# Kernel tuning notes

Hardware: AMD Instinct MI355X
Metric: run time of the kernel (lower is better)

Reference implementation:

```python
import jax, jax.numpy as jnp
import numpy as np

B, S, H, NH, M = 2, 2048, 1024, 16, 512  # batch, seq, hidden, heads, medical/clinical dim
D = H // NH
EPS = 1e-12


def setup_inputs() -> dict:
    key = jax.random.key(0)
    ks = jax.random.split(key, 20)
    sd = 0.02
    return {
        'hidden_states': jax.random.normal(ks[0], (B, S, H), jnp.float32),
        'medical_context': jax.random.normal(ks[1], (B, S, H), jnp.float32),
        'Wq': jax.random.normal(ks[2], (H, H), jnp.float32) * sd,
        'bq': jnp.zeros((H,), jnp.float32),
        'Wk': jax.random.normal(ks[3], (H, H), jnp.float32) * sd,
        'bk': jnp.zeros((H,), jnp.float32),
        'Wv': jax.random.normal(ks[4], (H, H), jnp.float32) * sd,
        'bv': jnp.zeros((H,), jnp.float32),
        'Wmq': jax.random.normal(ks[5], (H, M), jnp.float32) * sd,
        'bmq': jnp.zeros((M,), jnp.float32),
        'Wmk': jax.random.normal(ks[6], (H, M), jnp.float32) * sd,
        'bmk': jnp.zeros((M,), jnp.float32),
        'Wc': jax.random.normal(ks[7], (H, M), jnp.float32) * sd,
        'bc': jnp.zeros((M,), jnp.float32),
        'Wf': jax.random.normal(ks[8], (H + M, H), jnp.float32) * sd,
        'bf': jnp.zeros((H,), jnp.float32),
        'ln_g': jnp.ones((H,), jnp.float32),
        'ln_b': jnp.zeros((H,), jnp.float32),
    }


def _split_heads(x):  # [B,S,H] -> [B,NH,S,D]
    return x.reshape(B, S, NH, D).transpose(0, 2, 1, 3)


def reference(hidden_states, medical_context, Wq, bq, Wk, bk, Wv, bv,
              Wmq, bmq, Wmk, bmk, Wc, bc, Wf, bf, ln_g, ln_b):
    hs = hidden_states
    q = _split_heads(hs @ Wq + bq)
    k = _split_heads(hs @ Wk + bk)
    v = _split_heads(hs @ Wv + bv)
    scores = jnp.einsum('bhsd,bhtd->bhst', q, k) / jnp.sqrt(jnp.float32(D))
    # medical additive bias
    mq = hs @ Wmq + bmq                      # [B,S,M]
    mk = medical_context @ Wmk + bmk         # [B,S,M]
    med_scores = jax.nn.softmax(jnp.einsum('bsm,btm->bst', mq, mk), axis=-1)
    scores = scores + 0.3 * med_scores[:, None]
    probs = jax.nn.softmax(scores, axis=-1)  # [B,NH,S,S]
    ctx = jnp.einsum('bhst,bhtd->bhsd', probs, v)
    ctx = ctx.transpose(0, 2, 1, 3).reshape(B, S, H)
    clin = ctx @ Wc + bc                     # [B,S,M]
    ctx = jnp.concatenate([ctx, clin], axis=-1) @ Wf + bf
    x = ctx + hs
    mu = jnp.mean(x, axis=-1, keepdims=True)
    var = jnp.mean(jnp.square(x - mu), axis=-1, keepdims=True)
    out = (x - mu) / jnp.sqrt(var + EPS) * ln_g + ln_b
    return out, probs
```

## Files before the change

kernel.cpp:

```cpp
#include <hip/hip_runtime.h>
#include <hip/hip_bf16.h>
#include <cstddef>

#define B_   2
#define S_   2048
#define H_   1024
#define NH_  16
#define D_   64
#define M_   512
#define NTOK (B_*S_)

typedef __hip_bfloat16 bf16;
typedef __attribute__((ext_vector_type(8))) short bf16x8;
typedef __attribute__((ext_vector_type(4))) float f32x4;
typedef __attribute__((ext_vector_type(8))) unsigned short ushort8;

__device__ __forceinline__ float toF(bf16 x) { return __bfloat162float(x); }
__device__ __forceinline__ float bfbits2f(unsigned short s) { return __uint_as_float((unsigned)s << 16); }
__device__ __forceinline__ unsigned short f2bfbits(float f) {
    union { bf16 h; unsigned short s; } u; u.h = __float2bfloat16(f); return u.s;
}

__global__ __launch_bounds__(256)
void detect_dtype(const unsigned int* __restrict__ w, int* __restrict__ flag)
{
    __shared__ int cnt[256];
    const int tid = threadIdx.x;
    const unsigned int x = w[tid];
    const unsigned int e0 = (x >> 7) & 0xFFu;
    cnt[tid] = (e0 >= 100u && e0 <= 126u) ? 1 : 0;
    __syncthreads();
    for (int off = 128; off > 0; off >>= 1) {
        if (tid < off) cnt[tid] += cnt[tid + off];
        __syncthreads();
    }
    if (tid == 0) flag[0] = (cnt[0] >= 128) ? 1 : 0;
}

__global__ __launch_bounds__(256)
void convert_in(const void* __restrict__ src, float* __restrict__ dst, int n,
                const int* __restrict__ flag)
{
    const int isbf = *flag;
    for (int i = blockIdx.x * 256 + threadIdx.x; i < n; i += gridDim.x * 256)
        dst[i] = isbf ? toF(((const bf16*)src)[i]) : ((const float*)src)[i];
}

__global__ __launch_bounds__(256)
void to_bf16_pack(const float* __restrict__ src, unsigned int* __restrict__ dst,
                  int n2)
{
    int i = blockIdx.x * 256 + threadIdx.x;
    const int stride = gridDim.x * 256;
    for (; i < n2; i += stride) {
        const float2 f = ((const float2*)src)[i];
        const unsigned int lo = f2bfbits(f.x);
        const unsigned int hi = f2bfbits(f.y);
        dst[i] = lo | (hi << 16);
    }
}

__global__ __launch_bounds__(256)
void gemm_tn(const float* __restrict__ A, const float* __restrict__ W,
             const float* __restrict__ bias, float* __restrict__ C,
             int M, int N, int K, int accumulate)
{
    __shared__ float As[16][68];
    __shared__ float Bs[16][68];
    const int tid = threadIdx.x;
    const int tx = tid & 15, ty = tid >> 4;
    const int m0 = blockIdx.y * 64, n0 = blockIdx.x * 64;
    float acc[4][4] = {};

    for (int k0 = 0; k0 < K; k0 += 16) {
        {
            const int r  = tid >> 2;
            const int cg = (tid & 3) * 4;
            const float* ap = A + (size_t)(m0 + r) * K + (k0 + cg);
            #pragma unroll
            for (int j = 0; j < 4; ++j) As[cg + j][r] = ap[j];
        }
        {
            const int r  = tid >> 4;
            const int cg = (tid & 15) * 4;
            const float* wp = W + (size_t)(k0 + r) * N + (n0 + cg);
            #pragma unroll
            for (int j = 0; j < 4; ++j) Bs[r][cg + j] = wp[j];
        }
        __syncthreads();
        #pragma unroll
        for (int kk = 0; kk < 16; ++kk) {
            float a[4], b[4];
            #pragma unroll
            for (int i = 0; i < 4; ++i) a[i] = As[kk][ty * 4 + i];
            #pragma unroll
            for (int j = 0; j < 4; ++j) b[j] = Bs[kk][tx * 4 + j];
            #pragma unroll
            for (int i = 0; i < 4; ++i)
                #pragma unroll
                for (int j = 0; j < 4; ++j)
                    acc[i][j] += a[i] * b[j];
        }
        __syncthreads();
    }

    #pragma unroll
    for (int i = 0; i < 4; ++i) {
        const int row = m0 + ty * 4 + i;
        #pragma unroll
        for (int j = 0; j < 4; ++j) {
            const int col = n0 + tx * 4 + j;
            float v = acc[i][j];
            if (bias) v += bias[col];
            const size_t idx = (size_t)row * N + col;
            if (accumulate) C[idx] += v; else C[idx] = v;
        }
    }
}

__global__ __launch_bounds__(256)
void med_logits(const float* __restrict__ mq, const float* __restrict__ mk,
                float* __restrict__ out)
{
    const int b = blockIdx.z;
    const float* A  = mq + (size_t)b * S_ * M_;
    const float* Bm = mk + (size_t)b * S_ * M_;
    __shared__ float As[16][68];
    __shared__ float Bs[16][68];
    const int tid = threadIdx.x;
    const int tx = tid & 15, ty = tid >> 4;
    const int m0 = blockIdx.y * 64, n0 = blockIdx.x * 64;
    float acc[4][4] = {};

    for (int k0 = 0; k0 < M_; k0 += 16) {
        const int r  = tid >> 2;
        const int cg = (tid & 3) * 4;
        const float* ap = A  + (size_t)(m0 + r) * M_ + (k0 + cg);
        const float* bp = Bm + (size_t)(n0 + r) * M_ + (k0 + cg);
        #pragma unroll
        for (int j = 0; j < 4; ++j) { As[cg + j][r] = ap[j]; Bs[cg + j][r] = bp[j]; }
        __syncthreads();
        #pragma unroll
        for (int kk = 0; kk < 16; ++kk) {
            float a[4], b[4];
            #pragma unroll
            for (int i = 0; i < 4; ++i) a[i] = As[kk][ty * 4 + i];
            #pragma unroll
            for (int j = 0; j < 4; ++j) b[j] = Bs[kk][tx * 4 + j];
            #pragma unroll
            for (int i = 0; i < 4; ++i)
                #pragma unroll
                for (int j = 0; j < 4; ++j)
                    acc[i][j] += a[i] * b[j];
        }
        __syncthreads();
    }
    #pragma unroll
    for (int i = 0; i < 4; ++i)
        #pragma unroll
        for (int j = 0; j < 4; ++j)
            out[(size_t)b * S_ * S_ + (size_t)(m0 + ty * 4 + i) * S_ + (n0 + tx * 4 + j)]
                = acc[i][j];
}

__global__ __launch_bounds__(256)
void row_softmax(float* __restrict__ x)
{
    float* p = x + (size_t)blockIdx.x * S_;
    __shared__ float red[256];
    const int tid = threadIdx.x;

    float m = -1e30f;
    for (int i = tid; i < S_; i += 256) m = fmaxf(m, p[i]);
    red[tid] = m; __syncthreads();
    for (int off = 128; off > 0; off >>= 1) {
        if (tid < off) red[tid] = fmaxf(red[tid], red[tid + off]);
        __syncthreads();
    }
    const float mx = red[0];
    __syncthreads();

    float s = 0.f;
    for (int i = tid; i < S_; i += 256) {
        float e = __expf(fmaxf(p[i] - mx, -80.f));
        p[i] = e; s += e;
    }
    red[tid] = s; __syncthreads();
    for (int off = 128; off > 0; off >>= 1) {
        if (tid < off) red[tid] += red[tid + off];
        __syncthreads();
    }
    const float inv = 1.f / fmaxf(red[0], 1e-30f);
    for (int i = tid; i < S_; i += 256) p[i] *= inv;
}

__global__ __launch_bounds__(256)
void qk_scores(const bf16* __restrict__ qh, const bf16* __restrict__ kh,
               const float* __restrict__ medp, void* __restrict__ dout,
               const int* __restrict__ flag)
{
    const int isbf = *flag;
    const int bh = blockIdx.z;
    const int b = bh >> 4;
    const int s0 = blockIdx.y * 64;
    const int t0 = blockIdx.x * 64;
    const int tid  = threadIdx.x;
    const int wave = tid >> 6, lane = tid & 63;
    const int wr = (wave >> 1) * 32, wc = (wave & 1) * 32;
    const int lr = lane & 15;
    const int lk = (lane >> 4) * 8;
    const int h  = bh & 15;

    const bf16* qp = qh + (size_t)(b * S_ + s0 + wr + lr) * H_ + h * D_ + lk;
    const bf16* kp = kh + (size_t)(b * S_ + t0 + wc + lr) * H_ + h * D_ + lk;

    f32x4 acc00 = {0.f, 0.f, 0.f, 0.f};
    f32x4 acc01 = acc00, acc10 = acc00, acc11 = acc00;

    #pragma unroll
    for (int ks = 0; ks < 2; ++ks) {
        const int d = ks * 32;
        const bf16x8 a0 = *(const bf16x8*)(qp + d);
        const bf16x8 a1 = *(const bf16x8*)(qp + (size_t)16 * H_ + d);
        const bf16x8 b0 = *(const bf16x8*)(kp + d);
        const bf16x8 b1 = *(const bf16x8*)(kp + (size_t)16 * H_ + d);
        acc00 = __builtin_amdgcn_mfma_f32_16x16x32_bf16(a0, b0, acc00, 0, 0, 0);
        acc01 = __builtin_amdgcn_mfma_f32_16x16x32_bf16(a0, b1, acc01, 0, 0, 0);
        acc10 = __builtin_amdgcn_mfma_f32_16x16x32_bf16(a1, b0, acc10, 0, 0, 0);
        acc11 = __builtin_amdgcn_mfma_f32_16x16x32_bf16(a1, b1, acc11, 0, 0, 0);
    }

    const size_t pbase = (size_t)NTOK * H_ + ((size_t)bh * S_ + s0) * S_ + t0;
    bf16*  ob = (bf16*)dout  + pbase;
    float* of = (float*)dout + pbase;
    const int crow = (lane >> 4) * 4;
    const int ccol = lane & 15;

    #pragma unroll
    for (int ti = 0; ti < 2; ++ti) {
        const f32x4 aT0 = ti ? acc10 : acc00;
        const f32x4 aT1 = ti ? acc11 : acc01;
        #pragma unroll
        for (int r = 0; r < 4; ++r) {
            const int row = wr + ti * 16 + crow + r;
            const float* mrow = medp + ((size_t)b * S_ + s0 + row) * S_ + t0;
            {
                const int col = wc + ccol;
                const float v = aT0[r] * 0.125f + 0.3f * mrow[col];
                if (isbf) ob[(size_t)row * S_ + col] = __float2bfloat16(v);
                else      of[(size_t)row * S_ + col] = v;
            }
            {
                const int col = wc + 16 + ccol;
                const float v = aT1[r] * 0.125f + 0.3f * mrow[col];
                if (isbf) ob[(size_t)row * S_ + col] = __float2bfloat16(v);
                else      of[(size_t)row * S_ + col] = v;
            }
        }
    }
}

__global__ __launch_bounds__(256)
void prob_softmax(void* __restrict__ dout, const int* __restrict__ flag)
{
    const int isbf = *flag;
    const int tid = threadIdx.x;
    const size_t base = (size_t)NTOK * H_ + (size_t)blockIdx.x * S_;
    __shared__ float red[256];
    float x[8];
    bf16*  pb = (bf16*)dout  + base;
    float* pf = (float*)dout + base;

    if (isbf) {
        const ushort8 v = *(const ushort8*)(pb + tid * 8);
        #pragma unroll
        for (int j = 0; j < 8; ++j) x[j] = bfbits2f(v[j]);
    } else {
        const float4 f0 = ((const float4*)pf)[tid * 2];
        const float4 f1 = ((const float4*)pf)[tid * 2 + 1];
        x[0] = f0.x; x[1] = f0.y; x[2] = f0.z; x[3] = f0.w;
        x[4] = f1.x; x[5] = f1.y; x[6] = f1.z; x[7] = f1.w;
    }

    float m = x[0];
    #pragma unroll
    for (int j = 1; j < 8; ++j) m = fmaxf(m, x[j]);
    red[tid] = m; __syncthreads();
    for (int off = 128; off > 0; off >>= 1) {
        if (tid < off) red[tid] = fmaxf(red[tid], red[tid + off]);
        __syncthreads();
    }
    const float mx = red[0];
    __syncthreads();

    float s = 0.f;
    #pragma unroll
    for (int j = 0; j < 8; ++j) {
        x[j] = __expf(fmaxf(x[j] - mx, -80.f));
        s += x[j];
    }
    red[tid] = s; __syncthreads();
    for (int off = 128; off > 0; off >>= 1) {
        if (tid < off) red[tid] += red[tid + off];
        __syncthreads();
    }
    const float inv = 1.f / fmaxf(red[0], 1e-30f);

    if (isbf) {
        ushort8 v;
        #pragma unroll
        for (int j = 0; j < 8; ++j) v[j] = f2bfbits(x[j] * inv);
        *(ushort8*)(pb + tid * 8) = v;
    } else {
        float4 f0, f1;
        f0.x = x[0] * inv; f0.y = x[1] * inv; f0.z = x[2] * inv; f0.w = x[3] * inv;
        f1.x = x[4] * inv; f1.y = x[5] * inv; f1.z = x[6] * inv; f1.w = x[7] * inv;
        ((float4*)pf)[tid * 2]     = f0;
        ((float4*)pf)[tid * 2 + 1] = f1;
    }
}

__global__ __launch_bounds__(256)
void pv_gemm(const void* __restrict__ dout, const float* __restrict__ v,
             float* __restrict__ ctx, const int* __restrict__ flag)
{
    const int isbf = *flag;
    const int bh = blockIdx.y;
    const int b = bh >> 4, h = bh & 15;
    const int m0 = blockIdx.x * 64;
    const size_t pbase = (size_t)NTOK * H_ + (size_t)bh * S_ * S_;
    const bf16*  Ab = (const bf16*)dout  + pbase;
    const float* Af = (const float*)dout + pbase;
    const float* Bv = v + (size_t)b * S_ * H_ + h * D_;
    __shared__ float As[16][68];
    __shared__ float Bs[16][68];
    const int tid = threadIdx.x;
    const int tx = tid & 15, ty = tid >> 4;
    float acc[4][4] = {};

    for (int k0 = 0; k0 < S_; k0 += 16) {
        {
            const int r  = tid >> 2;
            const int cg = (tid & 3) * 4;
            const size_t base = (size_t)(m0 + r) * S_ + (k0 + cg);
            #pragma unroll
            for (int j = 0; j < 4; ++j)
                As[cg + j][r] = isbf ? toF(Ab[base + j]) : Af[base + j];
        }
        {
            const int r  = tid >> 4;
            const int cg = (tid & 15) * 4;
            const float* bp = Bv + (size_t)(k0 + r) * H_ + cg;
            #pragma unroll
            for (int j = 0; j < 4; ++j) Bs[r][cg + j] = bp[j];
        }
        __syncthreads();
        #pragma unroll
        for (int kk = 0; kk < 16; ++kk) {
            float a[4], bb[4];
            #pragma unroll
            for (int i = 0; i < 4; ++i) a[i]  = As[kk][ty * 4 + i];
            #pragma unroll
            for (int j = 0; j < 4; ++j) bb[j] = Bs[kk][tx * 4 + j];
            #pragma unroll
            for (int i = 0; i < 4; ++i)
                #pragma unroll
                for (int j = 0; j < 4; ++j)
                    acc[i][j] += a[i] * bb[j];
        }
        __syncthreads();
    }
    #pragma unroll
    for (int i = 0; i < 4; ++i)
        #pragma unroll
        for (int j = 0; j < 4; ++j)
            ctx[(size_t)(b * S_ + m0 + ty * 4 + i) * H_ + h * D_ + tx * 4 + j] = acc[i][j];
}

__global__ __launch_bounds__(256)
void add_ln(const float* __restrict__ f, const float* __restrict__ hs,
            const float* __restrict__ g, const float* __restrict__ bta,
            void* __restrict__ dout, const int* __restrict__ flag)
{
    const int isbf = *flag;
    const int row = blockIdx.x;
    const int tid = threadIdx.x;
    __shared__ float red[256];
    float x[4];
    #pragma unroll
    for (int i = 0; i < 4; ++i) {
        const int c = tid + i * 256;
        x[i] = f[(size_t)row * H_ + c] + hs[(size_t)row * H_ + c];
    }
    float s = x[0] + x[1] + x[2] + x[3];
    red[tid] = s; __syncthreads();
    for (int off = 128; off > 0; off >>= 1) {
        if (tid < off) red[tid] += red[tid + off];
        __syncthreads();
    }
    const float mu = red[0] * (1.f / (float)H_);
    __syncthreads();

    float vs = 0.f;
    #pragma unroll
    for (int i = 0; i < 4; ++i) { const float d = x[i] - mu; vs += d * d; }
    red[tid] = vs; __syncthreads();
    for (int off = 128; off > 0; off >>= 1) {
        if (tid < off) red[tid] += red[tid + off];
        __syncthreads();
    }
    const float var = red[0] * (1.f / (float)H_);
    const float inv = 1.f / sqrtf(var + 1e-12f);
    bf16*  ob = (bf16*)dout;
    float* of = (float*)dout;
    #pragma unroll
    for (int i = 0; i < 4; ++i) {
        const int c = tid + i * 256;
        const float y = (x[i] - mu) * inv * g[c] + bta[c];
        if (isbf) ob[(size_t)row * H_ + c] = __float2bfloat16(y);
        else      of[(size_t)row * H_ + c] = y;
    }
}

extern "C" void kernel_launch(void* const* d_in, const int* in_sizes, int n_in,
                              void* d_out, int out_size, void* d_ws, size_t ws_size,
                              hipStream_t stream)
{
    int* flag = (int*)d_ws;
    float* p = (float*)((char*)d_ws + 256);

    float* hs_f  = p; p += (size_t)NTOK * H_;
    float* mc_f  = p; p += (size_t)NTOK * H_;
    float* Wq_f  = p; p += (size_t)H_ * H_;
    float* Wk_f  = p; p += (size_t)H_ * H_;
    float* Wv_f  = p; p += (size_t)H_ * H_;
    float* Wmq_f = p; p += (size_t)H_ * M_;
    float* Wmk_f = p; p += (size_t)H_ * M_;
    float* Wc_f  = p; p += (size_t)H_ * M_;
    float* Wf_f  = p; p += (size_t)(H_ + M_) * H_;
    float* bq_f  = p; p += H_;
    float* bk_f  = p; p += H_;
    float* bv_f  = p; p += H_;
    float* bmq_f = p; p += M_;
    float* bmk_f = p; p += M_;
    float* bc_f  = p; p += M_;
    float* bf_f  = p; p += H_;
    float* lng_f = p; p += H_;
    float* lnb_f = p; p += H_;

    float* q    = p; p += (size_t)NTOK * H_;
    float* k    = p; p += (size_t)NTOK * H_;
    float* v    = p; p += (size_t)NTOK * H_;
    float* mq   = p; p += (size_t)NTOK * M_;
    float* mk   = p; p += (size_t)NTOK * M_;
    float* medp = p; p += (size_t)B_ * S_ * S_;
    float* ctx  = p; p += (size_t)NTOK * H_;
    float* clin = p; p += (size_t)NTOK * M_;
    float* fbuf = p; p += (size_t)NTOK * H_;

    bf16* qh = (bf16*)mc_f;
    bf16* kh = (bf16*)(mc_f + (size_t)NTOK * H_ / 2);

    const dim3 blk(256);

    detect_dtype<<<1, blk, 0, stream>>>((const unsigned int*)d_in[2], flag);

    float* dsts[18] = { hs_f, mc_f, Wq_f, bq_f, Wk_f, bk_f, Wv_f, bv_f,
                        Wmq_f, bmq_f, Wmk_f, bmk_f, Wc_f, bc_f, Wf_f, bf_f,
                        lng_f, lnb_f };
    for (int i = 0; i < 18; ++i) {
        const int n = in_sizes[i];
        const int g = (n + 255) / 256;
        convert_in<<<dim3(g > 1024 ? 1024 : g), blk, 0, stream>>>(d_in[i], dsts[i], n, flag);
    }

    gemm_tn<<<dim3(16, 64), blk, 0, stream>>>(hs_f, Wq_f, bq_f, q, NTOK, H_, H_, 0);
    gemm_tn<<<dim3(16, 64), blk, 0, stream>>>(hs_f, Wk_f, bk_f, k, NTOK, H_, H_, 0);
    gemm_tn<<<dim3(16, 64), blk, 0, stream>>>(hs_f, Wv_f, bv_f, v, NTOK, H_, H_, 0);
    gemm_tn<<<dim3(8, 64),  blk, 0, stream>>>(hs_f, Wmq_f, bmq_f, mq, NTOK, M_, H_, 0);
    gemm_tn<<<dim3(8, 64),  blk, 0, stream>>>(mc_f, Wmk_f, bmk_f, mk, NTOK, M_, H_, 0);

    to_bf16_pack<<<dim3(2048), blk, 0, stream>>>(q, (unsigned int*)qh, NTOK * H_ / 2);
    to_bf16_pack<<<dim3(2048), blk, 0, stream>>>(k, (unsigned int*)kh, NTOK * H_ / 2);

    med_logits<<<dim3(32, 32, 2), blk, 0, stream>>>(mq, mk, medp);
    row_softmax<<<dim3(B_ * S_), blk, 0, stream>>>(medp);

    qk_scores<<<dim3(32, 32, 32), blk, 0, stream>>>(qh, kh, medp, d_out, flag);
    prob_softmax<<<dim3(B_ * NH_ * S_), blk, 0, stream>>>(d_out, flag);

    pv_gemm<<<dim3(32, 32), blk, 0, stream>>>(d_out, v, ctx, flag);

    gemm_tn<<<dim3(8, 64),  blk, 0, stream>>>(ctx, Wc_f, bc_f, clin, NTOK, M_, H_, 0);
    gemm_tn<<<dim3(16, 64), blk, 0, stream>>>(ctx, Wf_f, bf_f, fbuf, NTOK, H_, H_, 0);
    gemm_tn<<<dim3(16, 64), blk, 0, stream>>>(clin, Wf_f + (size_t)H_ * H_, (const float*)nullptr,
                                              fbuf, NTOK, H_, M_, 1);

    add_ln<<<dim3(NTOK), blk, 0, stream>>>(fbuf, hs_f, lng_f, lnb_f, d_out, flag);
}
```

Measured before the change: 2.268 ms.

## Add bf16 MFMA path for all projection, medical and PV GEMMs

When inputs are detected as bf16, the weights are transposed to bf16 and every projection GEMM, the medical logits GEMM, the PV product and the output GEMMs run through MFMA kernels writing bf16 intermediates. The clin projection writes into a concatenated buffer so the final projection becomes a single GEMM. The old fp32 scalar path stays behind the flag for fp32 inputs. The goal is to replace slow fp32 SIMT GEMMs with matrix-core work and halve intermediate traffic, at the cost of extra transposes, no LDS reuse in the MFMA kernels, and bf16 rounding of intermediates.

```diff
diff --git a/kernel.cpp b/kernel.cpp
--- a/kernel.cpp
+++ b/kernel.cpp
@@ -48,23 +48,155 @@
 
 __global__ __launch_bounds__(256)
 void to_bf16_pack(const float* __restrict__ src, unsigned int* __restrict__ dst,
-                  int n2)
-{
+                  int n2, const int* __restrict__ flag)
+{
+    if (*flag) return;
     int i = blockIdx.x * 256 + threadIdx.x;
     const int stride = gridDim.x * 256;
     for (; i < n2; i += stride) {
         const float2 f = ((const float2*)src)[i];
-        const unsigned int lo = f2bfbits(f.x);
-        const unsigned int hi = f2bfbits(f.y);
-        dst[i] = lo | (hi << 16);
+        dst[i] = (unsigned)f2bfbits(f.x) | ((unsigned)f2bfbits(f.y) << 16);
+    }
+}
+
+__global__ __launch_bounds__(256)
+void transpose_bf16(const unsigned short* __restrict__ src,
+                    unsigned short* __restrict__ dst,
+                    int Kr, int Nc, const int* __restrict__ flag)
+{
+    if (*flag == 0) return;
+    __shared__ unsigned short t[64][72];
+    const int k0 = blockIdx.x * 64, n0 = blockIdx.y * 64;
+    const int tid = threadIdx.x;
+    const int r = tid >> 2, c = (tid & 3) * 16;
+    const ushort8 v0 = *(const ushort8*)(src + (size_t)(k0 + r) * Nc + n0 + c);
+    const ushort8 v1 = *(const ushort8*)(src + (size_t)(k0 + r) * Nc + n0 + c + 8);
+    #pragma unroll
+    for (int j = 0; j < 8; ++j) { t[r][c + j] = v0[j]; t[r][c + 8 + j] = v1[j]; }
+    __syncthreads();
+    ushort8 w0, w1;
+    #pragma unroll
+    for (int j = 0; j < 8; ++j) { w0[j] = t[c + j][r]; w1[j] = t[c + 8 + j][r]; }
+    *(ushort8*)(dst + (size_t)(n0 + r) * Kr + k0 + c)     = w0;
+    *(ushort8*)(dst + (size_t)(n0 + r) * Kr + k0 + c + 8) = w1;
+}
+
+__global__ __launch_bounds__(256)
+void gemm_mfma(const bf16* __restrict__ A, const bf16* __restrict__ Bt,
+               const float* __restrict__ bias, void* __restrict__ Cv,
+               const int* __restrict__ flag, int K,
+               int lda, int ldb, int ldc,
+               size_t sAz, size_t sBz, size_t sCz, int out_bf16)
+{
+    if (*flag == 0) return;
+    const int z = blockIdx.z;
+    const int m0 = blockIdx.y * 64, n0 = blockIdx.x * 64;
+    const int tid = threadIdx.x, wave = tid >> 6, lane = tid & 63;
+    const int wr = (wave >> 1) * 32, wc = (wave & 1) * 32;
+    const int lr = lane & 15, lk = (lane >> 4) * 8;
+
+    const bf16* ap = A  + (size_t)z * sAz + (size_t)(m0 + wr + lr) * lda + lk;
+    const bf16* bp = Bt + (size_t)z * sBz + (size_t)(n0 + wc + lr) * ldb + lk;
+
+    f32x4 acc00 = {0.f, 0.f, 0.f, 0.f};
+    f32x4 acc01 = acc00, acc10 = acc00, acc11 = acc00;
+
+    for (int k0 = 0; k0 < K; k0 += 64) {
+        #pragma unroll
+        for (int u = 0; u < 2; ++u) {
+            const int d = k0 + u * 32;
+            const bf16x8 a0 = *(const bf16x8*)(ap + d);
+            const bf16x8 a1 = *(const bf16x8*)(ap + (size_t)16 * lda + d);
+            const bf16x8 b0 = *(const bf16x8*)(bp + d);
+            const bf16x8 b1 = *(const bf16x8*)(bp + (size_t)16 * ldb + d);
+            acc00 = __builtin_amdgcn_mfma_f32_16x16x32_bf16(a0, b0, acc00, 0, 0, 0);
+            acc01 = __builtin_amdgcn_mfma_f32_16x16x32_bf16(a0, b1, acc01, 0, 0, 0);
+            acc10 = __builtin_amdgcn_mfma_f32_16x16x32_bf16(a1, b0, acc10, 0, 0, 0);
+            acc11 = __builtin_amdgcn_mfma_f32_16x16x32_bf16(a1, b1, acc11, 0, 0, 0);
+        }
+    }
+
+    const int crow = (lane >> 4) * 4, ccol = lane & 15;
+    const size_t cbase = (size_t)z * sCz;
+    #pragma unroll
+    for (int ti = 0; ti < 2; ++ti) {
+        const f32x4 A0 = ti ? acc10 : acc00;
+        const f32x4 A1 = ti ? acc11 : acc01;
+        #pragma unroll
+        for (int r = 0; r < 4; ++r) {
+            const int row = m0 + wr + ti * 16 + crow + r;
+            const int c0 = n0 + wc + ccol;
+            const int c1 = c0 + 16;
+            float v0 = A0[r], v1 = A1[r];
+            if (bias) { v0 += bias[c0]; v1 += bias[c1]; }
+            const size_t i0 = cbase + (size_t)row * ldc + c0;
+            const size_t i1 = cbase + (size_t)row * ldc + c1;
+            if (out_bf16) {
+                ((bf16*)Cv)[i0] = __float2bfloat16(v0);
+                ((bf16*)Cv)[i1] = __float2bfloat16(v1);
+            } else {
+                ((float*)Cv)[i0] = v0;
+                ((float*)Cv)[i1] = v1;
+            }
+        }
+    }
+}
+
+__global__ __launch_bounds__(256)
+void pv_mfma(const void* __restrict__ dout, const bf16* __restrict__ vhT,
+             bf16* __restrict__ cat, const int* __restrict__ flag)
+{
+    if (*flag == 0) return;
+    const int bh = blockIdx.z;
+    const int b = bh >> 4, h = bh & 15;
+    const int m0 = blockIdx.x * 64;
+    const int tid = threadIdx.x, wave = tid >> 6, lane = tid & 63;
+    const int wr = (wave >> 1) * 32, wc = (wave & 1) * 32;
+    const int lr = lane & 15, lk = (lane >> 4) * 8;
+
+    const bf16* P  = (const bf16*)dout + (size_t)NTOK * H_ + (size_t)bh * S_ * S_;
+    const bf16* ap = P + (size_t)(m0 + wr + lr) * S_ + lk;
+    const bf16* bp = vhT + (size_t)(h * 64 + wc + lr) * (size_t)NTOK + (size_t)b * S_ + lk;
+
+    f32x4 acc00 = {0.f, 0.f, 0.f, 0.f};
+    f32x4 acc01 = acc00, acc10 = acc00, acc11 = acc00;
+
+    for (int k0 = 0; k0 < S_; k0 += 64) {
+        #pragma unroll
+        for (int u = 0; u < 2; ++u) {
+            const int d = k0 + u * 32;
+            const bf16x8 a0 = *(const bf16x8*)(ap + d);
+            const bf16x8 a1 = *(const bf16x8*)(ap + (size_t)16 * S_ + d);
+            const bf16x8 b0 = *(const bf16x8*)(bp + d);
+            const bf16x8 b1 = *(const bf16x8*)(bp + (size_t)16 * NTOK + d);
+            acc00 = __builtin_amdgcn_mfma_f32_16x16x32_bf16(a0, b0, acc00, 0, 0, 0);
+            acc01 = __builtin_amdgcn_mfma_f32_16x16x32_bf16(a0, b1, acc01, 0, 0, 0);
+            acc10 = __builtin_amdgcn_mfma_f32_16x16x32_bf16(a1, b0, acc10, 0, 0, 0);
+            acc11 = __builtin_amdgcn_mfma_f32_16x16x32_bf16(a1, b1, acc11, 0, 0, 0);
+        }
+    }
+
+    const int crow = (lane >> 4) * 4, ccol = lane & 15;
+    #pragma unroll
+    for (int ti = 0; ti < 2; ++ti) {
+        const f32x4 A0 = ti ? acc10 : acc00;
+        const f32x4 A1 = ti ? acc11 : acc01;
+        #pragma unroll
+        for (int r = 0; r < 4; ++r) {
+            const int rowl = m0 + wr + ti * 16 + crow + r;
+            const size_t rbase = (size_t)(b * S_ + rowl) * (H_ + M_) + h * 64;
+            cat[rbase + wc + ccol]      = __float2bfloat16(A0[r]);
+            cat[rbase + wc + 16 + ccol] = __float2bfloat16(A1[r]);
+        }
     }
 }
 
 __global__ __launch_bounds__(256)
 void gemm_tn(const float* __restrict__ A, const float* __restrict__ W,
              const float* __restrict__ bias, float* __restrict__ C,
-             int M, int N, int K, int accumulate)
-{
+             int M, int N, int K, int accumulate, const int* __restrict__ flag)
+{
+    if (*flag != 0) return;
     __shared__ float As[16][68];
     __shared__ float Bs[16][68];
     const int tid = threadIdx.x;
@@ -120,8 +252,9 @@
 
 __global__ __launch_bounds__(256)
 void med_logits(const float* __restrict__ mq, const float* __restrict__ mk,
-                float* __restrict__ out)
-{
+                float* __restrict__ out, const int* __restrict__ flag)
+{
+    if (*flag != 0) return;
     const int b = blockIdx.z;
     const float* A  = mq + (size_t)b * S_ * M_;
     const float* Bm = mk + (size_t)b * S_ * M_;
@@ -164,8 +297,9 @@
 }
 
 __global__ __launch_bounds__(256)
-void row_softmax(float* __restrict__ x)
-{
+void row_softmax(float* __restrict__ x, const int* __restrict__ flag)
+{
+    if (*flag != 0) return;
     float* p = x + (size_t)blockIdx.x * S_;
     __shared__ float red[256];
     const int tid = threadIdx.x;
@@ -195,9 +329,50 @@
 }
 
 __global__ __launch_bounds__(256)
+void med_softmax_bf16(const float* __restrict__ in, unsigned short* __restrict__ out,
+                      const int* __restrict__ flag)
+{
+    if (*flag == 0) return;
+    const int tid = threadIdx.x;
+    const float* p = in + (size_t)blockIdx.x * S_;
+    unsigned short* o = out + (size_t)blockIdx.x * S_;
+    __shared__ float red[256];
+    float x[8];
+    const float4 f0 = ((const float4*)p)[tid * 2];
+    const float4 f1 = ((const float4*)p)[tid * 2 + 1];
+    x[0]=f0.x; x[1]=f0.y; x[2]=f0.z; x[3]=f0.w;
+    x[4]=f1.x; x[5]=f1.y; x[6]=f1.z; x[7]=f1.w;
+
+    float m = x[0];
+    #pragma unroll
+    for (int j = 1; j < 8; ++j) m = fmaxf(m, x[j]);
+    red[tid] = m; __syncthreads();
+    for (int off = 128; off > 0; off >>= 1) {
+        if (tid < off) red[tid] = fmaxf(red[tid], red[tid + off]);
+        __syncthreads();
+    }
+    const float mx = red[0];
+    __syncthreads();
+
+    float s = 0.f;
+    #pragma unroll
+    for (int j = 0; j < 8; ++j) { x[j] = __expf(fmaxf(x[j] - mx, -80.f)); s += x[j]; }
+    red[tid] = s; __syncthreads();
+    for (int off = 128; off > 0; off >>= 1) {
+        if (tid < off) red[tid] += red[tid + off];
+        __syncthreads();
+    }
+    const float inv = 1.f / fmaxf(red[0], 1e-30f);
+    ushort8 v;
+    #pragma unroll
+    for (int j = 0; j < 8; ++j) v[j] = f2bfbits(x[j] * inv);
+    *(ushort8*)(o + tid * 8) = v;
+}
+
+__global__ __launch_bounds__(256)
 void qk_scores(const bf16* __restrict__ qh, const bf16* __restrict__ kh,
-               const float* __restrict__ medp, void* __restrict__ dout,
-               const int* __restrict__ flag)
+               const float* __restrict__ medf, const unsigned short* __restrict__ medh,
+               void* __restrict__ dout, const int* __restrict__ flag)
 {
     const int isbf = *flag;
     const int bh = blockIdx.z;
@@ -243,16 +418,18 @@
         #pragma unroll
         for (int r = 0; r < 4; ++r) {
             const int row = wr + ti * 16 + crow + r;
-            const float* mrow = medp + ((size_t)b * S_ + s0 + row) * S_ + t0;
+            const size_t mrow = ((size_t)b * S_ + s0 + row) * S_ + t0;
             {
                 const int col = wc + ccol;
-                const float v = aT0[r] * 0.125f + 0.3f * mrow[col];
+                const float mv = isbf ? bfbits2f(medh[mrow + col]) : medf[mrow + col];
+                const float v = aT0[r] * 0.125f + 0.3f * mv;
                 if (isbf) ob[(size_t)row * S_ + col] = __float2bfloat16(v);
                 else      of[(size_t)row * S_ + col] = v;
             }
             {
                 const int col = wc + 16 + ccol;
-                const float v = aT1[r] * 0.125f + 0.3f * mrow[col];
+                const float mv = isbf ? bfbits2f(medh[mrow + col]) : medf[mrow + col];
+                const float v = aT1[r] * 0.125f + 0.3f * mv;
                 if (isbf) ob[(size_t)row * S_ + col] = __float2bfloat16(v);
                 else      of[(size_t)row * S_ + col] = v;
             }
@@ -324,12 +501,11 @@
 void pv_gemm(const void* __restrict__ dout, const float* __restrict__ v,
              float* __restrict__ ctx, const int* __restrict__ flag)
 {
-    const int isbf = *flag;
+    if (*flag != 0) return;
     const int bh = blockIdx.y;
     const int b = bh >> 4, h = bh & 15;
     const int m0 = blockIdx.x * 64;
     const size_t pbase = (size_t)NTOK * H_ + (size_t)bh * S_ * S_;
-    const bf16*  Ab = (const bf16*)dout  + pbase;
     const float* Af = (const float*)dout + pbase;
     const float* Bv = v + (size_t)b * S_ * H_ + h * D_;
     __shared__ float As[16][68];
@@ -344,8 +520,7 @@
             const int cg = (tid & 3) * 4;
             const size_t base = (size_t)(m0 + r) * S_ + (k0 + cg);
             #pragma unroll
-            for (int j = 0; j < 4; ++j)
-                As[cg + j][r] = isbf ? toF(Ab[base + j]) : Af[base + j];
+            for (int j = 0; j < 4; ++j) As[cg + j][r] = Af[base + j];
         }
         {
             const int r  = tid >> 4;
@@ -458,8 +633,21 @@
     float* clin = p; p += (size_t)NTOK * M_;
     float* fbuf = p; p += (size_t)NTOK * H_;
 
-    bf16* qh = (bf16*)mc_f;
-    bf16* kh = (bf16*)(mc_f + (size_t)NTOK * H_ / 2);
+    bf16* qh   = (bf16*)mc_f;
+    bf16* kh   = (bf16*)mc_f + (size_t)NTOK * H_;
+    bf16* vh   = (bf16*)q;
+    bf16* vhT  = (bf16*)q + (size_t)NTOK * H_;
+    bf16* mqh  = (bf16*)v;
+    bf16* mkh  = (bf16*)v + (size_t)NTOK * M_;
+    bf16* WcT  = (bf16*)v + (size_t)2 * NTOK * M_;
+    bf16* WfT  = WcT + (size_t)M_ * H_;
+    unsigned short* medp_h = (unsigned short*)mq;
+    bf16* cat  = (bf16*)ctx;
+    bf16* WqT  = (bf16*)clin;
+    bf16* WkT  = WqT + (size_t)H_ * H_;
+    bf16* WvT  = WkT + (size_t)H_ * H_;
+    bf16* WmqT = WvT + (size_t)H_ * H_;
+    bf16* WmkT = WmqT + (size_t)M_ * H_;
 
     const dim3 blk(256);
 
@@ -474,27 +662,57 @@
         convert_in<<<dim3(g > 1024 ? 1024 : g), blk, 0, stream>>>(d_in[i], dsts[i], n, flag);
     }
 
-    gemm_tn<<<dim3(16, 64), blk, 0, stream>>>(hs_f, Wq_f, bq_f, q, NTOK, H_, H_, 0);
-    gemm_tn<<<dim3(16, 64), blk, 0, stream>>>(hs_f, Wk_f, bk_f, k, NTOK, H_, H_, 0);
-    gemm_tn<<<dim3(16, 64), blk, 0, stream>>>(hs_f, Wv_f, bv_f, v, NTOK, H_, H_, 0);
-    gemm_tn<<<dim3(8, 64),  blk, 0, stream>>>(hs_f, Wmq_f, bmq_f, mq, NTOK, M_, H_, 0);
-    gemm_tn<<<dim3(8, 64),  blk, 0, stream>>>(mc_f, Wmk_f, bmk_f, mk, NTOK, M_, H_, 0);
-
-    to_bf16_pack<<<dim3(2048), blk, 0, stream>>>(q, (unsigned int*)qh, NTOK * H_ / 2);
-    to_bf16_pack<<<dim3(2048), blk, 0, stream>>>(k, (unsigned int*)kh, NTOK * H_ / 2);
-
-    med_logits<<<dim3(32, 32, 2), blk, 0, stream>>>(mq, mk, medp);
-    row_softmax<<<dim3(B_ * S_), blk, 0, stream>>>(medp);
-
-    qk_scores<<<dim3(32, 32, 32), blk, 0, stream>>>(qh, kh, medp, d_out, flag);
+    transpose_bf16<<<dim3(16, 16), blk, 0, stream>>>((const unsigned short*)d_in[2],  (unsigned short*)WqT,  H_, H_, flag);
+    transpose_bf16<<<dim3(16, 16), blk, 0, stream>>>((const unsigned short*)d_in[4],  (unsigned short*)WkT,  H_, H_, flag);
+    transpose_bf16<<<dim3(16, 16), blk, 0, stream>>>((const unsigned short*)d_in[6],  (unsigned short*)WvT,  H_, H_, flag);
+    transpose_bf16<<<dim3(16, 8),  blk, 0, stream>>>((const unsigned short*)d_in[8],  (unsigned short*)WmqT, H_, M_, flag);
+    transpose_bf16<<<dim3(16, 8),  blk, 0, stream>>>((const unsigned short*)d_in[10], (unsigned short*)WmkT, H_, M_, flag);
+    transpose_bf16<<<dim3(16, 8),  blk, 0, stream>>>((const unsigned short*)d_in[12], (unsigned short*)WcT,  H_, M_, flag);
+    transpose_bf16<<<dim3(24, 16), blk, 0, stream>>>((const unsigned short*)d_in[14], (unsigned short*)WfT,  H_ + M_, H_, flag);
+
+    gemm_mfma<<<dim3(16, 64, 1), blk, 0, stream>>>((const bf16*)d_in[0], WqT, bq_f, qh, flag,
+                                                   H_, H_, H_, H_, 0, 0, 0, 1);
+    gemm_mfma<<<dim3(16, 64, 1), blk, 0, stream>>>((const bf16*)d_in[0], WkT, bk_f, kh, flag,
+                                                   H_, H_, H_, H_, 0, 0, 0, 1);
+    gemm_mfma<<<dim3(16, 64, 1), blk, 0, stream>>>((const bf16*)d_in[0], WvT, bv_f, vh, flag,
+                                                   H_, H_, H_, H_, 0, 0, 0, 1);
+    gemm_mfma<<<dim3(8, 64, 1),  blk, 0, stream>>>((const bf16*)d_in[0], WmqT, bmq_f, mqh, flag,
+                                                   H_, H_, H_, M_, 0, 0, 0, 1);
+    gemm_mfma<<<dim3(8, 64, 1),  blk, 0, stream>>>((const bf16*)d_in[1], WmkT, bmk_f, mkh, flag,
+                                                   H_, H_, H_, M_, 0, 0, 0, 1);
+    transpose_bf16<<<dim3(64, 16), blk, 0, stream>>>((const unsigned short*)vh, (unsigned short*)vhT,
+                                                     NTOK, H_, flag);
+
+    gemm_tn<<<dim3(16, 64), blk, 0, stream>>>(hs_f, Wq_f, bq_f, q, NTOK, H_, H_, 0, flag);
+    gemm_tn<<<dim3(16, 64), blk, 0, stream>>>(hs_f, Wk_f, bk_f, k, NTOK, H_, H_, 0, flag);
+    gemm_tn<<<dim3(16, 64), blk, 0, stream>>>(hs_f, Wv_f, bv_f, v, NTOK, H_, H_, 0, flag);
+    gemm_tn<<<dim3(8, 64),  blk, 0, stream>>>(hs_f, Wmq_f, bmq_f, mq, NTOK, M_, H_, 0, flag);
+    gemm_tn<<<dim3(8, 64),  blk, 0, stream>>>(mc_f, Wmk_f, bmk_f, mk, NTOK, M_, H_, 0, flag);
+    to_bf16_pack<<<dim3(2048), blk, 0, stream>>>(q, (unsigned int*)qh, NTOK * H_ / 2, flag);
+    to_bf16_pack<<<dim3(2048), blk, 0, stream>>>(k, (unsigned int*)kh, NTOK * H_ / 2, flag);
+
+    gemm_mfma<<<dim3(32, 32, 2), blk, 0, stream>>>(mqh, mkh, (const float*)nullptr, medp, flag,
+                                                   M_, M_, M_, S_,
+                                                   (size_t)S_ * M_, (size_t)S_ * M_,
+                                                   (size_t)S_ * S_, 0);
+    med_logits<<<dim3(32, 32, 2), blk, 0, stream>>>(mq, mk, medp, flag);
+    med_softmax_bf16<<<dim3(B_ * S_), blk, 0, stream>>>(medp, medp_h, flag);
+    row_softmax<<<dim3(B_ * S_), blk, 0, stream>>>(medp, flag);
+
+    qk_scores<<<dim3(32, 32, 32), blk, 0, stream>>>(qh, kh, medp, medp_h, d_out, flag);
     prob_softmax<<<dim3(B_ * NH_ * S_), blk, 0, stream>>>(d_out, flag);
 
+    pv_mfma<<<dim3(32, 1, 32), blk, 0, stream>>>(d_out, vhT, cat, flag);
     pv_gemm<<<dim3(32, 32), blk, 0, stream>>>(d_out, v, ctx, flag);
 
-    gemm_tn<<<dim3(8, 64),  blk, 0, stream>>>(ctx, Wc_f, bc_f, clin, NTOK, M_, H_, 0);
-    gemm_tn<<<dim3(16, 64), blk, 0, stream>>>(ctx, Wf_f, bf_f, fbuf, NTOK, H_, H_, 0);
+    gemm_mfma<<<dim3(8, 64, 1), blk, 0, stream>>>(cat, WcT, bc_f, cat + H_, flag,
+                                                  H_, H_ + M_, H_, H_ + M_, 0, 0, 0, 1);
+    gemm_mfma<<<dim3(16, 64, 1), blk, 0, stream>>>(cat, WfT, bf_f, fbuf, flag,
+                                                   H_ + M_, H_ + M_, H_ + M_, H_, 0, 0, 0, 0);
+    gemm_tn<<<dim3(8, 64),  blk, 0, stream>>>(ctx, Wc_f, bc_f, clin, NTOK, M_, H_, 0, flag);
+    gemm_tn<<<dim3(16, 64), blk, 0, stream>>>(ctx, Wf_f, bf_f, fbuf, NTOK, H_, H_, 0, flag);
     gemm_tn<<<dim3(16, 64), blk, 0, stream>>>(clin, Wf_f + (size_t)H_ * H_, (const float*)nullptr,
-                                              fbuf, NTOK, H_, M_, 1);
+                                              fbuf, NTOK, H_, M_, 1, flag);
 
     add_ln<<<dim3(NTOK), blk, 0, stream>>>(fbuf, hs_f, lng_f, lnb_f, d_out, flag);
 }
```

Measured after the change: 2.166 ms. -4.5%, faster.
